# Optimization experiments

Measured on AMD Instinct MI355X. Metric: run time of the kernel, lower is better.

Reference implementation:

```python
import jax, jax.numpy as jnp
import numpy as np
from jax import lax

D_MODEL = 96; D_STATE = 16; D_INNER = 192; DT_RANK = 6; K = 4
BSZ = 2; HH = 64; WW = 64


def setup_inputs() -> dict:
    key = jax.random.key(0)
    ks = jax.random.split(key, 16)
    f = lambda k, shape, s=0.02: (jax.random.normal(k, shape) * s).astype(jnp.float32)
    P = DT_RANK + 2 * D_STATE
    return {
        "x": jax.random.normal(ks[0], (BSZ, HH, WW, D_MODEL), jnp.float32),
        "W_in": f(ks[1], (2 * D_INNER, D_MODEL)),
        "b_in": jnp.zeros((2 * D_INNER,), jnp.float32),
        "conv_w": f(ks[2], (D_INNER, 1, 3, 3)),
        "conv_b": jnp.zeros((D_INNER,), jnp.float32),
        "W_xp": f(ks[3], (K * P, K * D_INNER)),
        "b_xp": jnp.zeros((K * P,), jnp.float32),
        "W_dt": f(ks[4], (K * D_INNER, K * DT_RANK)),
        "b_dt": f(ks[5], (K * D_INNER,), 0.1),
        "A_log": jax.random.normal(ks[6], (K * D_INNER, D_STATE), jnp.float32),
        "D_skip": jnp.ones((K * D_INNER,), jnp.float32),
        "dt_bias": jax.random.normal(ks[7], (K * D_INNER,), jnp.float32),
        "W_out": f(ks[8], (D_MODEL, D_INNER)),
        "b_out": jnp.zeros((D_MODEL,), jnp.float32),
        "gamma": jnp.ones((D_INNER,), jnp.float32),
        "beta": jnp.zeros((D_INNER,), jnp.float32),
    }


def cross_scan(x):
    # x: (B, D, H, W) -> (B, 4, D, L); dirs: row-major, col-major, and their reverses
    B, D, H, W = x.shape
    L = H * W
    x0 = x.reshape(B, D, L)
    x1 = jnp.swapaxes(x, 2, 3).reshape(B, D, L)
    return jnp.stack([x0, x1, x0[..., ::-1], x1[..., ::-1]], axis=1)


def cross_merge(ys):
    # ys: (B, 4, D, H, W) -> (B, D, L); inverse of cross_scan, summed
    B, Kk, D, H, W = ys.shape
    L = H * W
    yf = ys.reshape(B, Kk, D, L)
    y02 = yf[:, 0] + yf[:, 2, :, ::-1]
    y13 = yf[:, 1] + yf[:, 3, :, ::-1]
    y13 = jnp.swapaxes(y13.reshape(B, D, W, H), 2, 3).reshape(B, D, L)
    return y02 + y13


def selective_scan(u, dt, A, Bm, Cm, D_skip, dt_bias):
    # u, dt: (B,K,Dv,L); A: (K,Dv,N); Bm, Cm: (B,K,N,L); D_skip, dt_bias: (K,Dv)
    # NOTE: torch code repeats Bm/Cm across Dv; we broadcast instead (same math).
    dt = jax.nn.softplus(dt + dt_bias[None, :, :, None])
    dt_l = jnp.moveaxis(dt, -1, 0)   # (L,B,K,Dv)
    u_l = jnp.moveaxis(u, -1, 0)     # (L,B,K,Dv)
    B_l = jnp.moveaxis(Bm, -1, 0)    # (L,B,K,N)
    C_l = jnp.moveaxis(Cm, -1, 0)    # (L,B,K,N)

    def step(h, inp):
        dt_t, u_t, b_t, c_t = inp
        dA = jnp.exp(dt_t[..., None] * A[None])                 # (B,K,Dv,N)
        dBu = (dt_t * u_t)[..., None] * b_t[:, :, None, :]      # (B,K,Dv,N)
        h = dA * h + dBu
        y = jnp.einsum('bkdn,bkn->bkd', h, c_t)
        return h, y

    h0 = jnp.zeros(u.shape[:3] + (A.shape[-1],), u.dtype)
    _, ys = lax.scan(step, h0, (dt_l, u_l, B_l, C_l))
    ys = jnp.moveaxis(ys, 0, -1)  # (B,K,Dv,L)
    return ys + u * D_skip[None, :, :, None]


def reference(x, W_in, b_in, conv_w, conv_b, W_xp, b_xp, W_dt, b_dt,
              A_log, D_skip, dt_bias, W_out, b_out, gamma, beta):
    B, H, W, _ = x.shape
    L = H * W
    xz = x @ W_in.T + b_in
    xx, z = jnp.split(xz, 2, axis=-1)
    z = jax.nn.silu(z)
    xc = jnp.transpose(xx, (0, 3, 1, 2))  # (B, D, H, W)
    xc = lax.conv_general_dilated(xc, conv_w, (1, 1), 'SAME',
                                  feature_group_count=D_INNER,
                                  dimension_numbers=('NCHW', 'OIHW', 'NCHW'))
    xc = jax.nn.silu(xc + conv_b[None, :, None, None])

    xs = cross_scan(xc)                      # (B, K, D, L)
    xs_flat = xs.reshape(B, K * D_INNER, L)

    x_dbl = jnp.einsum('bcl,pc->bpl', xs_flat, W_xp) + b_xp[None, :, None]
    x_dbl = x_dbl.reshape(B, K, DT_RANK + 2 * D_STATE, L)
    dts, Bm, Cm = jnp.split(x_dbl, [DT_RANK, DT_RANK + D_STATE], axis=2)
    dts = dts.reshape(B, K * DT_RANK, L)
    dts = jnp.einsum('brl,dr->bdl', dts, W_dt) + b_dt[None, :, None]

    A = -jnp.exp(A_log).reshape(K, D_INNER, D_STATE)
    u = xs_flat.reshape(B, K, D_INNER, L)
    dt = dts.reshape(B, K, D_INNER, L)
    ys = selective_scan(u, dt, A, Bm, Cm,
                        D_skip.reshape(K, D_INNER), dt_bias.reshape(K, D_INNER))

    y = cross_merge(ys.reshape(B, K, D_INNER, H, W))  # (B, D, L)
    y = jnp.transpose(y.reshape(B, D_INNER, H, W), (0, 2, 3, 1))

    mu = jnp.mean(y, axis=-1, keepdims=True)
    var = jnp.mean(jnp.square(y - mu), axis=-1, keepdims=True)
    y = (y - mu) * lax.rsqrt(var + 1e-5) * gamma + beta
    y = y * z
    return y @ W_out.T + b_out
```

## Files before the change

### kernel.cpp

```cpp
#include <hip/hip_runtime.h>
#include <cstdint>
#include <cstddef>


#define CHUNK 16
#define NCK   256

#if __has_builtin(__builtin_amdgcn_exp2f)
#define EXP2(x) __builtin_amdgcn_exp2f(x)
#else
#define EXP2(x) exp2f(x)
#endif
#define LOG2E 1.44269504088896340736f
#define LN2   0.69314718055994530942f

typedef __attribute__((ext_vector_type(8))) short short8;
typedef __attribute__((ext_vector_type(8))) unsigned short ushort8;
typedef __attribute__((ext_vector_type(4))) float f32x4;

__device__ __forceinline__ float siluf(float x){ return x * (1.f/(1.f+__expf(-x))); }
__device__ __forceinline__ float softplus_fast(float v){
  float e  = EXP2(v*LOG2E);
  float sp = LN2*__log2f(1.f + e);
  return (v > 20.f) ? v : sp;
}
__device__ __forceinline__ unsigned short f2b(float f){
  uint32_t u = __float_as_uint(f);
  uint32_t r = (u + 0x7fffu + ((u>>16)&1u)) >> 16;
  return (unsigned short)r;
}
__device__ __forceinline__ short8 cast8(const float* p){
  float4 f0 = *(const float4*)p;
  float4 f1 = *(const float4*)(p+4);
  unsigned short t[8] = {f2b(f0.x),f2b(f0.y),f2b(f0.z),f2b(f0.w),
                         f2b(f1.x),f2b(f1.y),f2b(f1.z),f2b(f1.w)};
  return *(short8*)t;
}

__global__ __launch_bounds__(256) void k_pack(
    const float* __restrict__ Wxp, const float* __restrict__ Win,
    const float* __restrict__ Wout,
    unsigned short* __restrict__ Wf, unsigned short* __restrict__ Wfin,
    unsigned short* __restrict__ Wfout)
{
  int tid = blockIdx.x*256 + threadIdx.x;
  int lane = tid & 63;
  int n = lane & 15, q = lane >> 4;
  if (tid < 18432){
    int rest = tid >> 6;
    int pt = rest % 6; rest /= 6;
    int k32 = rest & 3; rest >>= 2;
    int kc = rest % 6; int ph = rest / 6;
    int p = ph*96 + pt*16 + n;
    int kbase = kc*128 + k32*32 + q*8;
    unsigned short v[8];
#pragma unroll
    for (int j = 0; j < 8; j++)
      v[j] = (p < 152) ? f2b(Wxp[(size_t)p*768 + kbase + j]) : (unsigned short)0;
    *(ushort8*)(Wf + (size_t)tid*8) = *(ushort8*)v;
  } else if (tid < 23040){
    int e = tid - 18432;
    int rest = e >> 6;
    int nt = rest % 24, k32 = rest / 24;
    int p = nt*16 + n;
    int kbase = k32*32 + q*8;
    unsigned short v[8];
#pragma unroll
    for (int j = 0; j < 8; j++) v[j] = f2b(Win[(size_t)p*96 + kbase + j]);
    *(ushort8*)(Wfin + (size_t)e*8) = *(ushort8*)v;
  } else if (tid < 25344){
    int e = tid - 23040;
    int rest = e >> 6;
    int nt = rest % 6, k32 = rest / 6;
    int p = nt*16 + n;
    int kbase = k32*32 + q*8;
    unsigned short v[8];
#pragma unroll
    for (int j = 0; j < 8; j++) v[j] = f2b(Wout[(size_t)p*192 + kbase + j]);
    *(ushort8*)(Wfout + (size_t)e*8) = *(ushort8*)v;
  }
}

__global__ __launch_bounds__(256) void k_gemm_in(
    const float* __restrict__ x, const unsigned short* __restrict__ Wfin,
    const float* __restrict__ bias, float* __restrict__ xx, float* __restrict__ zs)
{
  const int tid = threadIdx.x;
  const int lane = tid & 63, w = tid >> 6;
  const int m0 = blockIdx.x*32;
  const int n = lane & 15, q = lane >> 4;
  f32x4 acc[2][6] = {};
#pragma unroll
  for (int k32 = 0; k32 < 3; k32++){
    int kb = k32*32 + q*8;
    short8 a[2];
#pragma unroll
    for (int mf = 0; mf < 2; mf++)
      a[mf] = cast8(x + (size_t)(m0 + mf*16 + n)*96 + kb);
#pragma unroll
    for (int j = 0; j < 6; j++){
      int nt = w*6 + j;
      short8 bfr = *(const short8*)(Wfin + ((size_t)(k32*24 + nt)*64 + lane)*8);
#pragma unroll
      for (int mf = 0; mf < 2; mf++)
        acc[mf][j] = __builtin_amdgcn_mfma_f32_16x16x32_bf16(a[mf], bfr, acc[mf][j], 0, 0, 0);
    }
  }
#pragma unroll
  for (int mf = 0; mf < 2; mf++)
#pragma unroll
    for (int j = 0; j < 6; j++){
      int nn = w*96 + j*16 + n;
      float bv = bias[nn];
#pragma unroll
      for (int reg = 0; reg < 4; reg++){
        int l = m0 + mf*16 + q*4 + reg;
        float v = acc[mf][j][reg] + bv;
        if (nn < 192) xx[(size_t)l*192 + nn] = v;
        else          zs[(size_t)l*192 + (nn-192)] = siluf(v);
      }
    }
}

__global__ __launch_bounds__(256) void k_conv(
    const float* __restrict__ xx, const float* __restrict__ cw, const float* __restrict__ cb,
    float* __restrict__ xc,
    unsigned short* __restrict__ xcb, unsigned short* __restrict__ xcTb)
{
  int gid = blockIdx.x*256 + threadIdx.x;
  int c = gid % 192;
  int l = (gid/192) & 4095;
  int b = gid / (192*4096);
  int h = l >> 6, w = l & 63;
  float s = 0.f;
#pragma unroll
  for (int kh = 0; kh < 3; kh++){
    int h2 = h + kh - 1;
    if ((unsigned)h2 >= 64u) continue;
#pragma unroll
    for (int kw = 0; kw < 3; kw++){
      int w2 = w + kw - 1;
      if ((unsigned)w2 >= 64u) continue;
      s += xx[((size_t)b*4096 + h2*64 + w2)*192 + c] * cw[c*9 + kh*3 + kw];
    }
  }
  s = siluf(s + cb[c]);
  unsigned short sb = f2b(s);
  size_t i0 = ((size_t)b*4096 + l)*192 + c;
  xc[i0] = s; xcb[i0] = sb;
  int tl = (l & 63)*64 + (l >> 6);
  xcTb[((size_t)b*4096 + tl)*192 + c] = sb;
}

__global__ __launch_bounds__(256) void k_gemm_xdbl(
    const unsigned short* __restrict__ xcb, const unsigned short* __restrict__ xcTb,
    const unsigned short* __restrict__ Wf, const float* __restrict__ bxp,
    float* __restrict__ xdbl, float* __restrict__ dts_c)
{
  __shared__ unsigned short Bsh[4*6*64*8];
  const int tid = threadIdx.x;
  const int lane = tid & 63, w = tid >> 6;
  const int wl = w & 1, wp = w >> 1;
  const int l0 = blockIdx.x*64, ph = blockIdx.y, b = blockIdx.z;
  const int n = lane & 15, q = lane >> 4;
  f32x4 acc[2][3] = {};
  const unsigned short* slab0 = Wf + (size_t)ph*6*12288;
  for (int kc = 0; kc < 6; kc++){
    __syncthreads();
    const ushort8* srcp = (const ushort8*)(slab0 + (size_t)kc*12288);
#pragma unroll
    for (int t = 0; t < 6; t++) ((ushort8*)Bsh)[tid + t*256] = srcp[tid + t*256];
    __syncthreads();
#pragma unroll
    for (int k32 = 0; k32 < 4; k32++){
      int kk = kc*128 + k32*32;
      int dir = kk/192; int ch = kk%192 + q*8;
      const unsigned short* sp = (dir & 1) ? xcTb : xcb;
      bool rev = (dir >= 2);
      short8 a[2];
#pragma unroll
      for (int mt = 0; mt < 2; mt++){
        int ls = l0 + wl*32 + mt*16 + n;
        int row = rev ? 4095 - ls : ls;
        a[mt] = *(const short8*)(sp + ((size_t)b*4096 + row)*192 + ch);
      }
#pragma unroll
      for (int j = 0; j < 3; j++){
        short8 bfr = *(const short8*)&Bsh[((size_t)(k32*6 + wp*3 + j)*64 + lane)*8];
#pragma unroll
        for (int mt = 0; mt < 2; mt++)
          acc[mt][j] = __builtin_amdgcn_mfma_f32_16x16x32_bf16(a[mt], bfr, acc[mt][j], 0, 0, 0);
      }
    }
  }
#pragma unroll
  for (int mt = 0; mt < 2; mt++)
#pragma unroll
    for (int j = 0; j < 3; j++){
      int p = ph*96 + (wp*3+j)*16 + n;
      if (p < 152){
        int k = p/38, pp = p%38;
        int off = (pp < 6) ? pp : pp + 2;
        float bias = bxp[p];
#pragma unroll
        for (int reg = 0; reg < 4; reg++){
          int l = l0 + wl*32 + mt*16 + q*4 + reg;
          float val = acc[mt][j][reg] + bias;
          xdbl[(((size_t)b*4 + k)*4096 + l)*48 + off] = val;
          if (pp < 6) dts_c[((size_t)b*4096 + l)*24 + k*6 + pp] = val;
        }
      }
    }
}

__global__ __launch_bounds__(256) void k_scanA(
    const float* __restrict__ xc, const float* __restrict__ xdbl,
    const float* __restrict__ dts_c,
    const float* __restrict__ A_log, const float* __restrict__ Wdt,
    const float* __restrict__ bdt, const float* __restrict__ dtbias,
    const float* __restrict__ Dskip,
    float* __restrict__ ylcs, float* __restrict__ sdtb, float* __restrict__ Sb)
{
  const int lane = threadIdx.x & 63;
  const int wid  = __builtin_amdgcn_readfirstlane(blockIdx.x*4 + (threadIdx.x >> 6));
  const int ck = wid & (NCK-1); const int g = wid / NCK;
  const int dblk = g % 3; const int bk = g / 3;
  const int k = bk & 3; const int b = bk >> 2;
  const int d = dblk*64 + lane; const int ch = k*192 + d;
  float An[16];
  {
    const float4* ap = (const float4*)(A_log + (size_t)ch*16);
#pragma unroll
    for (int i = 0; i < 4; i++){
      float4 t = ap[i];
      An[4*i+0] = -LOG2E*__expf(t.x); An[4*i+1] = -LOG2E*__expf(t.y);
      An[4*i+2] = -LOG2E*__expf(t.z); An[4*i+3] = -LOG2E*__expf(t.w);
    }
  }
  float Wr[24];
#pragma unroll
  for (int r = 0; r < 24; r++) Wr[r] = Wdt[(size_t)ch*24 + r];
  const float bsum = bdt[ch] + dtbias[ch];
  const float Dv = Dskip[ch];
  const int l0 = ck*CHUNK;
  const bool rev = (k >= 2);
  const int tr = k & 1;
  const int T0 = tr ? ((l0 & 63)*64 + (l0 >> 6)) : l0;
  const int rs = tr ? 64 : 1;
  const int row0 = rev ? 4095 - T0 : T0;
  const int rstep = (rev ? -rs : rs)*192;
  const float* up  = xc + ((size_t)b*4096 + row0)*192 + d;
  const float* qc  = dts_c + ((size_t)b*4096 + l0)*24;
  const float* xbc = xdbl + (((size_t)b*4 + k)*4096 + l0)*48;
  float* ylp = ylcs + ((((size_t)b*4 + k)*4096 + l0)*192 + d)*2;
  float h[16];
#pragma unroll
  for (int n = 0; n < 16; n++) h[n] = 0.f;
  float sdt = 0.f;
#pragma unroll 4
  for (int t = 0; t < CHUNK; t++){
    float u  = up[0];
    float4 B0 = *(const float4*)(xbc + 8);
    float4 B1 = *(const float4*)(xbc + 12);
    float4 B2 = *(const float4*)(xbc + 16);
    float4 B3 = *(const float4*)(xbc + 20);
    float4 C0 = *(const float4*)(xbc + 24);
    float4 C1 = *(const float4*)(xbc + 28);
    float4 C2 = *(const float4*)(xbc + 32);
    float4 C3 = *(const float4*)(xbc + 36);
    float Bv[16] = {B0.x,B0.y,B0.z,B0.w, B1.x,B1.y,B1.z,B1.w,
                    B2.x,B2.y,B2.z,B2.w, B3.x,B3.y,B3.z,B3.w};
    float Cv[16] = {C0.x,C0.y,C0.z,C0.w, C1.x,C1.y,C1.z,C1.w,
                    C2.x,C2.y,C2.z,C2.w, C3.x,C3.y,C3.z,C3.w};
    float4 q0 = *(const float4*)(qc);
    float4 q1 = *(const float4*)(qc + 4);
    float4 q2 = *(const float4*)(qc + 8);
    float4 q3 = *(const float4*)(qc + 12);
    float4 q4 = *(const float4*)(qc + 16);
    float4 q5 = *(const float4*)(qc + 20);
    float qv[24] = {q0.x,q0.y,q0.z,q0.w, q1.x,q1.y,q1.z,q1.w,
                    q2.x,q2.y,q2.z,q2.w, q3.x,q3.y,q3.z,q3.w,
                    q4.x,q4.y,q4.z,q4.w, q5.x,q5.y,q5.z,q5.w};
    float v0 = bsum, v1 = 0.f, v2 = 0.f, v3 = 0.f;
#pragma unroll
    for (int r = 0; r < 24; r += 4){
      v0 = fmaf(Wr[r+0], qv[r+0], v0);
      v1 = fmaf(Wr[r+1], qv[r+1], v1);
      v2 = fmaf(Wr[r+2], qv[r+2], v2);
      v3 = fmaf(Wr[r+3], qv[r+3], v3);
    }
    float dt = softplus_fast((v0+v1) + (v2+v3));
    float dtu = dt*u;
    sdt += dt;
    float y0 = u*Dv;
    float y1 = 0.f;
#pragma unroll
    for (int n = 0; n < 16; n += 2){
      float dA0 = EXP2(dt*An[n]);
      float dA1 = EXP2(dt*An[n+1]);
      h[n]   = fmaf(dA0, h[n],   dtu*Bv[n]);
      h[n+1] = fmaf(dA1, h[n+1], dtu*Bv[n+1]);
      y0 = fmaf(h[n],   Cv[n],   y0);
      y1 = fmaf(h[n+1], Cv[n+1], y1);
    }
    *(float2*)ylp = make_float2(y0 + y1, sdt);
    qc += 24; xbc += 48; up += rstep; ylp += 384;
  }
  size_t base = ((size_t)wid*16)*64 + lane;
  sdtb[(size_t)wid*64 + lane] = sdt;
#pragma unroll
  for (int n = 0; n < 16; n++) Sb[base + n*64] = h[n];
}

__global__ __launch_bounds__(64) void k_scanB(
    const float* __restrict__ A_log, const float* __restrict__ sdtb,
    const float* __restrict__ Sb, float* __restrict__ H0)
{
  int tid = blockIdx.x*64 + threadIdx.x;
  int lane = tid & 63; int n = (tid >> 6) & 15; int g = tid >> 10;
  int dblk = g % 3; int bk = g / 3; int k = bk & 3;
  int ch = k*192 + dblk*64 + lane;
  float An = -LOG2E*__expf(A_log[(size_t)ch*16 + n]);
  float h = 0.f;
#pragma unroll 8
  for (int ck = 0; ck < NCK; ck++){
    size_t sidx = ((size_t)(g*NCK + ck))*64 + lane;
    size_t idx  = (((size_t)(g*NCK + ck)*16) + n)*64 + lane;
    H0[idx] = h;
    h = fmaf(EXP2(An*sdtb[sidx]), h, Sb[idx]);
  }
}

__global__ __launch_bounds__(256) void k_scanC(
    const float* __restrict__ xdbl, const float* __restrict__ A_log,
    const float* __restrict__ ylcs, const float* __restrict__ H0,
    float* __restrict__ ys)
{
  const int lane = threadIdx.x & 63;
  const int wid  = __builtin_amdgcn_readfirstlane(blockIdx.x*4 + (threadIdx.x >> 6));
  const int ck = wid & (NCK-1); const int g = wid / NCK;
  const int dblk = g % 3; const int bk = g / 3;
  const int k = bk & 3; const int b = bk >> 2;
  const int d = dblk*64 + lane; const int ch = k*192 + d;
  float An[16];
  {
    const float4* ap = (const float4*)(A_log + (size_t)ch*16);
#pragma unroll
    for (int i = 0; i < 4; i++){
      float4 t = ap[i];
      An[4*i+0] = -LOG2E*__expf(t.x); An[4*i+1] = -LOG2E*__expf(t.y);
      An[4*i+2] = -LOG2E*__expf(t.z); An[4*i+3] = -LOG2E*__expf(t.w);
    }
  }
  const int l0 = ck*CHUNK;
  const bool rev = (k >= 2);
  const int tr = k & 1;
  const int T0 = tr ? ((l0 & 63)*64 + (l0 >> 6)) : l0;
  const int rs = tr ? 64 : 1;
  const int row0 = rev ? 4095 - T0 : T0;
  const int rstep = (rev ? -rs : rs)*192;
  const float* xbc = xdbl + (((size_t)b*4 + k)*4096 + l0)*48;
  const float* ylp = ylcs + ((((size_t)b*4 + k)*4096 + l0)*192 + d)*2;
  float* ysp = ys + ((size_t)(k*2 + b))*4096*192 + (size_t)row0*192 + d;
  float h0r[16];
  size_t base = ((size_t)wid*16)*64 + lane;
#pragma unroll
  for (int n = 0; n < 16; n++) h0r[n] = H0[base + n*64];
#pragma unroll 4
  for (int t = 0; t < CHUNK; t++){
    float2 yc = *(const float2*)ylp;
    float4 C0 = *(const float4*)(xbc + 24);
    float4 C1 = *(const float4*)(xbc + 28);
    float4 C2 = *(const float4*)(xbc + 32);
    float4 C3 = *(const float4*)(xbc + 36);
    float Cv[16] = {C0.x,C0.y,C0.z,C0.w, C1.x,C1.y,C1.z,C1.w,
                    C2.x,C2.y,C2.z,C2.w, C3.x,C3.y,C3.z,C3.w};
    float cs = yc.y;
    float y0 = yc.x, y1 = 0.f;
#pragma unroll
    for (int n = 0; n < 16; n += 2){
      float e0 = EXP2(An[n]*cs)   * h0r[n];
      float e1 = EXP2(An[n+1]*cs) * h0r[n+1];
      y0 = fmaf(Cv[n],   e0, y0);
      y1 = fmaf(Cv[n+1], e1, y1);
    }
    ysp[0] = y0 + y1;
    ylp += 384; xbc += 48; ysp += rstep;
  }
}

__global__ __launch_bounds__(256) void k_lngemm(
    const float* __restrict__ ys, const float* __restrict__ zs,
    const float* __restrict__ gamma, const float* __restrict__ beta,
    const unsigned short* __restrict__ Wfout, const float* __restrict__ bout,
    float* __restrict__ out)
{
  __shared__ unsigned short Ash[32*200];
  const int tid = threadIdx.x;
  {
    const int row_l = tid >> 3, o = tid & 7;
    const int row = blockIdx.x*32 + row_l;
    const int b = row >> 12, l = row & 4095;
    const int c0 = o*24;
    float s[24];
#pragma unroll
    for (int j = 0; j < 6; j++){
      float sx = 0.f, sy = 0.f, sz = 0.f, sw = 0.f;
#pragma unroll
      for (int k = 0; k < 4; k++){
        float4 t = *(const float4*)(ys + (((size_t)(k*2+b))*4096 + l)*192 + c0 + j*4);
        sx += t.x; sy += t.y; sz += t.z; sw += t.w;
      }
      s[j*4+0]=sx; s[j*4+1]=sy; s[j*4+2]=sz; s[j*4+3]=sw;
    }
    float tot = 0.f;
#pragma unroll
    for (int j = 0; j < 24; j++) tot += s[j];
#pragma unroll
    for (int off = 1; off < 8; off <<= 1) tot += __shfl_xor(tot, off);
    float mean = tot*(1.f/192.f);
    float vs = 0.f;
#pragma unroll
    for (int j = 0; j < 24; j++){ s[j] -= mean; vs = fmaf(s[j], s[j], vs); }
#pragma unroll
    for (int off = 1; off < 8; off <<= 1) vs += __shfl_xor(vs, off);
    float rstd = rsqrtf(vs*(1.f/192.f) + 1e-5f);
    unsigned short vb[24];
#pragma unroll
    for (int j = 0; j < 6; j++){
      float4 g4 = *(const float4*)(gamma + c0 + j*4);
      float4 b4 = *(const float4*)(beta  + c0 + j*4);
      float4 z4 = *(const float4*)(zs + (size_t)row*192 + c0 + j*4);
      vb[j*4+0] = f2b((s[j*4+0]*rstd*g4.x + b4.x)*z4.x);
      vb[j*4+1] = f2b((s[j*4+1]*rstd*g4.y + b4.y)*z4.y);
      vb[j*4+2] = f2b((s[j*4+2]*rstd*g4.z + b4.z)*z4.z);
      vb[j*4+3] = f2b((s[j*4+3]*rstd*g4.w + b4.w)*z4.w);
    }
#pragma unroll
    for (int j = 0; j < 3; j++)
      *(ushort8*)(Ash + row_l*200 + c0 + j*8) = *(ushort8*)(vb + j*8);
  }
  __syncthreads();
  const int lane = tid & 63, w = tid >> 6;
  const int wm = w & 1, wn = w >> 1;
  const int n = lane & 15, q = lane >> 4;
  const int m0 = blockIdx.x*32 + wm*16;
  f32x4 acc[3] = {};
#pragma unroll
  for (int k32 = 0; k32 < 6; k32++){
    int kb = k32*32 + q*8;
    short8 a = *(const short8*)(Ash + (wm*16 + n)*200 + kb);
#pragma unroll
    for (int j = 0; j < 3; j++){
      int nt = wn*3 + j;
      short8 bfr = *(const short8*)(Wfout + ((size_t)(k32*6 + nt)*64 + lane)*8);
      acc[j] = __builtin_amdgcn_mfma_f32_16x16x32_bf16(a, bfr, acc[j], 0, 0, 0);
    }
  }
#pragma unroll
  for (int j = 0; j < 3; j++){
    int nn = wn*48 + j*16 + n;
    float bv = bout[nn];
#pragma unroll
    for (int reg = 0; reg < 4; reg++){
      int m = m0 + q*4 + reg;
      out[(size_t)m*96 + nn] = acc[j][reg] + bv;
    }
  }
}

extern "C" void kernel_launch(void* const* d_in, const int* in_sizes, int n_in,
                              void* d_out, int out_size, void* d_ws, size_t ws_size,
                              hipStream_t stream)
{
  const float* x      = (const float*)d_in[0];
  const float* W_in   = (const float*)d_in[1];
  const float* b_in   = (const float*)d_in[2];
  const float* conv_w = (const float*)d_in[3];
  const float* conv_b = (const float*)d_in[4];
  const float* W_xp   = (const float*)d_in[5];
  const float* b_xp   = (const float*)d_in[6];
  const float* W_dt   = (const float*)d_in[7];
  const float* b_dt   = (const float*)d_in[8];
  const float* A_log  = (const float*)d_in[9];
  const float* D_skip = (const float*)d_in[10];
  const float* dt_bias= (const float*)d_in[11];
  const float* W_out  = (const float*)d_in[12];
  const float* b_out  = (const float*)d_in[13];
  const float* gamma  = (const float*)d_in[14];
  const float* beta   = (const float*)d_in[15];
  float* out = (float*)d_out;

  float* ws    = (float*)d_ws;
  float* xx    = ws;
  float* zs    = ws + 1572864;
  float* xc    = ws + 3145728;
  float* xdbl  = ws + 4718592;
  float* ysb   = ws + 6291456;
  float* Sb    = ws + 12582912;
  float* H0    = ws + 18874368;
  float* sdtb  = ws + 25165824;
  float* dts_c = ws + 25559040;
  float* ylcs  = ws + 25755648;
  unsigned short* xcb   = (unsigned short*)(ws + 38338560);
  unsigned short* xcTb  = xcb + 1572864;
  unsigned short* Wf    = (unsigned short*)(ws + 39911424);
  unsigned short* Wfin  = (unsigned short*)(ws + 39985152);
  unsigned short* Wfout = (unsigned short*)(ws + 40003584);

  k_pack     <<<99,             256, 0, stream>>>(W_xp, W_in, W_out, Wf, Wfin, Wfout);
  k_gemm_in  <<<256,            256, 0, stream>>>(x, Wfin, b_in, xx, zs);
  k_conv     <<<6144,           256, 0, stream>>>(xx, conv_w, conv_b, xc, xcb, xcTb);
  k_gemm_xdbl<<<dim3(64, 2, 2), 256, 0, stream>>>(xcb, xcTb, Wf, b_xp, xdbl, dts_c);
  k_scanA    <<<1536,           256, 0, stream>>>(xc, xdbl, dts_c, A_log, W_dt, b_dt, dt_bias, D_skip, ylcs, sdtb, Sb);
  k_scanB    <<<384,            64,  0, stream>>>(A_log, sdtb, Sb, H0);
  k_scanC    <<<1536,           256, 0, stream>>>(xdbl, A_log, ylcs, H0, ysb);
  k_lngemm   <<<256,            256, 0, stream>>>(ysb, zs, gamma, beta, Wfout, b_out, out);
}
```

Baseline: 207.3 us.

## Split chunk-state scan into two-level span scan, vectorize conv, halve xdbl tile

The serial 256-step carry scan over chunk states becomes a two-level scan. First, 8 spans of 32 chunks are scanned in parallel, recording local prefix states and cumulative dt. Then a short 8-step pass over span totals runs, and scanC combines the two with exp(A*cum_dt). The depthwise conv now processes 4 channels per thread with float4 loads and vector stores. The xdbl GEMM tile shrinks to 32 rows for more blocks. The scan change trades a long serial dependency for an extra kernel launch and extra workspace traffic.

```diff
diff --git a/kernel.cpp b/kernel.cpp
--- a/kernel.cpp
+++ b/kernel.cpp
@@ -5,6 +5,8 @@
 
 #define CHUNK 16
 #define NCK   256
+#define SPAN  32
+#define NSP   8
 
 #if __has_builtin(__builtin_amdgcn_exp2f)
 #define EXP2(x) __builtin_amdgcn_exp2f(x)
@@ -128,11 +130,11 @@
     unsigned short* __restrict__ xcb, unsigned short* __restrict__ xcTb)
 {
   int gid = blockIdx.x*256 + threadIdx.x;
-  int c = gid % 192;
-  int l = (gid/192) & 4095;
-  int b = gid / (192*4096);
+  int c4 = gid % 48; int c = c4*4;
+  int l = (gid/48) & 4095;
+  int b = gid / (48*4096);
   int h = l >> 6, w = l & 63;
-  float s = 0.f;
+  float sx = 0.f, sy = 0.f, sz = 0.f, sw = 0.f;
 #pragma unroll
   for (int kh = 0; kh < 3; kh++){
     int h2 = h + kh - 1;
@@ -141,15 +143,24 @@
     for (int kw = 0; kw < 3; kw++){
       int w2 = w + kw - 1;
       if ((unsigned)w2 >= 64u) continue;
-      s += xx[((size_t)b*4096 + h2*64 + w2)*192 + c] * cw[c*9 + kh*3 + kw];
-    }
-  }
-  s = siluf(s + cb[c]);
-  unsigned short sb = f2b(s);
+      float4 v = *(const float4*)(xx + ((size_t)b*4096 + h2*64 + w2)*192 + c);
+      int o = kh*3 + kw;
+      sx = fmaf(v.x, cw[(c+0)*9 + o], sx);
+      sy = fmaf(v.y, cw[(c+1)*9 + o], sy);
+      sz = fmaf(v.z, cw[(c+2)*9 + o], sz);
+      sw = fmaf(v.w, cw[(c+3)*9 + o], sw);
+    }
+  }
+  float4 cbv = *(const float4*)(cb + c);
+  float4 s;
+  s.x = siluf(sx + cbv.x); s.y = siluf(sy + cbv.y);
+  s.z = siluf(sz + cbv.z); s.w = siluf(sw + cbv.w);
+  unsigned short sb[4] = {f2b(s.x), f2b(s.y), f2b(s.z), f2b(s.w)};
   size_t i0 = ((size_t)b*4096 + l)*192 + c;
-  xc[i0] = s; xcb[i0] = sb;
+  *(float4*)(xc + i0) = s;
+  *(uint2*)(xcb + i0) = *(uint2*)sb;
   int tl = (l & 63)*64 + (l >> 6);
-  xcTb[((size_t)b*4096 + tl)*192 + c] = sb;
+  *(uint2*)(xcTb + ((size_t)b*4096 + tl)*192 + c) = *(uint2*)sb;
 }
 
 __global__ __launch_bounds__(256) void k_gemm_xdbl(
@@ -161,9 +172,9 @@
   const int tid = threadIdx.x;
   const int lane = tid & 63, w = tid >> 6;
   const int wl = w & 1, wp = w >> 1;
-  const int l0 = blockIdx.x*64, ph = blockIdx.y, b = blockIdx.z;
+  const int l0 = blockIdx.x*32, ph = blockIdx.y, b = blockIdx.z;
   const int n = lane & 15, q = lane >> 4;
-  f32x4 acc[2][3] = {};
+  f32x4 acc[3] = {};
   const unsigned short* slab0 = Wf + (size_t)ph*6*12288;
   for (int kc = 0; kc < 6; kc++){
     __syncthreads();
@@ -177,40 +188,32 @@
       int dir = kk/192; int ch = kk%192 + q*8;
       const unsigned short* sp = (dir & 1) ? xcTb : xcb;
       bool rev = (dir >= 2);
-      short8 a[2];
-#pragma unroll
-      for (int mt = 0; mt < 2; mt++){
-        int ls = l0 + wl*32 + mt*16 + n;
-        int row = rev ? 4095 - ls : ls;
-        a[mt] = *(const short8*)(sp + ((size_t)b*4096 + row)*192 + ch);
-      }
+      int ls = l0 + wl*16 + n;
+      int row = rev ? 4095 - ls : ls;
+      short8 a = *(const short8*)(sp + ((size_t)b*4096 + row)*192 + ch);
 #pragma unroll
       for (int j = 0; j < 3; j++){
         short8 bfr = *(const short8*)&Bsh[((size_t)(k32*6 + wp*3 + j)*64 + lane)*8];
-#pragma unroll
-        for (int mt = 0; mt < 2; mt++)
-          acc[mt][j] = __builtin_amdgcn_mfma_f32_16x16x32_bf16(a[mt], bfr, acc[mt][j], 0, 0, 0);
+        acc[j] = __builtin_amdgcn_mfma_f32_16x16x32_bf16(a, bfr, acc[j], 0, 0, 0);
       }
     }
   }
 #pragma unroll
-  for (int mt = 0; mt < 2; mt++)
-#pragma unroll
-    for (int j = 0; j < 3; j++){
-      int p = ph*96 + (wp*3+j)*16 + n;
-      if (p < 152){
-        int k = p/38, pp = p%38;
-        int off = (pp < 6) ? pp : pp + 2;
-        float bias = bxp[p];
-#pragma unroll
-        for (int reg = 0; reg < 4; reg++){
-          int l = l0 + wl*32 + mt*16 + q*4 + reg;
-          float val = acc[mt][j][reg] + bias;
-          xdbl[(((size_t)b*4 + k)*4096 + l)*48 + off] = val;
-          if (pp < 6) dts_c[((size_t)b*4096 + l)*24 + k*6 + pp] = val;
-        }
+  for (int j = 0; j < 3; j++){
+    int p = ph*96 + (wp*3+j)*16 + n;
+    if (p < 152){
+      int k = p/38, pp = p%38;
+      int off = (pp < 6) ? pp : pp + 2;
+      float bias = bxp[p];
+#pragma unroll
+      for (int reg = 0; reg < 4; reg++){
+        int l = l0 + wl*16 + q*4 + reg;
+        float val = acc[j][reg] + bias;
+        xdbl[(((size_t)b*4 + k)*4096 + l)*48 + off] = val;
+        if (pp < 6) dts_c[((size_t)b*4096 + l)*24 + k*6 + pp] = val;
       }
     }
+  }
 }
 
 __global__ __launch_bounds__(256) void k_scanA(
@@ -312,9 +315,38 @@
   for (int n = 0; n < 16; n++) Sb[base + n*64] = h[n];
 }
 
-__global__ __launch_bounds__(64) void k_scanB(
+__global__ __launch_bounds__(256) void k_scanB1(
     const float* __restrict__ A_log, const float* __restrict__ sdtb,
-    const float* __restrict__ Sb, float* __restrict__ H0)
+    const float* __restrict__ Sb,
+    float* __restrict__ H0loc, float* __restrict__ cloc,
+    float* __restrict__ SpanS, float* __restrict__ SpanC)
+{
+  int tid = blockIdx.x*256 + threadIdx.x;
+  int lane = tid & 63; int n = (tid >> 6) & 15;
+  int span = (tid >> 10) & (NSP-1); int g = tid >> 13;
+  int dblk = g % 3; int bk = g / 3; int k = bk & 3;
+  int ch = k*192 + dblk*64 + lane;
+  float An = -LOG2E*__expf(A_log[(size_t)ch*16 + n]);
+  float h = 0.f, cs = 0.f;
+  int wid0 = g*NCK + span*SPAN;
+#pragma unroll 8
+  for (int c = 0; c < SPAN; c++){
+    size_t sidx = ((size_t)(wid0 + c))*64 + lane;
+    size_t idx  = (((size_t)(wid0 + c)*16) + n)*64 + lane;
+    H0loc[idx] = h;
+    if (n == 0) cloc[sidx] = cs;
+    float sd = sdtb[sidx];
+    h = fmaf(EXP2(An*sd), h, Sb[idx]);
+    cs += sd;
+  }
+  size_t sp = (size_t)(g*NSP + span);
+  SpanS[(sp*16 + n)*64 + lane] = h;
+  if (n == 0) SpanC[sp*64 + lane] = cs;
+}
+
+__global__ __launch_bounds__(64) void k_scanB2(
+    const float* __restrict__ A_log, const float* __restrict__ SpanS,
+    const float* __restrict__ SpanC, float* __restrict__ H0span)
 {
   int tid = blockIdx.x*64 + threadIdx.x;
   int lane = tid & 63; int n = (tid >> 6) & 15; int g = tid >> 10;
@@ -322,18 +354,20 @@
   int ch = k*192 + dblk*64 + lane;
   float An = -LOG2E*__expf(A_log[(size_t)ch*16 + n]);
   float h = 0.f;
-#pragma unroll 8
-  for (int ck = 0; ck < NCK; ck++){
-    size_t sidx = ((size_t)(g*NCK + ck))*64 + lane;
-    size_t idx  = (((size_t)(g*NCK + ck)*16) + n)*64 + lane;
-    H0[idx] = h;
-    h = fmaf(EXP2(An*sdtb[sidx]), h, Sb[idx]);
+#pragma unroll
+  for (int span = 0; span < NSP; span++){
+    size_t sp = (size_t)(g*NSP + span);
+    size_t idx = (sp*16 + n)*64 + lane;
+    H0span[idx] = h;
+    h = fmaf(EXP2(An*SpanC[sp*64 + lane]), h, SpanS[idx]);
   }
 }
 
 __global__ __launch_bounds__(256) void k_scanC(
     const float* __restrict__ xdbl, const float* __restrict__ A_log,
-    const float* __restrict__ ylcs, const float* __restrict__ H0,
+    const float* __restrict__ ylcs,
+    const float* __restrict__ H0loc, const float* __restrict__ cloc,
+    const float* __restrict__ H0span,
     float* __restrict__ ys)
 {
   const int lane = threadIdx.x & 63;
@@ -363,9 +397,16 @@
   const float* ylp = ylcs + ((((size_t)b*4 + k)*4096 + l0)*192 + d)*2;
   float* ysp = ys + ((size_t)(k*2 + b))*4096*192 + (size_t)row0*192 + d;
   float h0r[16];
-  size_t base = ((size_t)wid*16)*64 + lane;
-#pragma unroll
-  for (int n = 0; n < 16; n++) h0r[n] = H0[base + n*64];
+  {
+    size_t base = ((size_t)wid*16)*64 + lane;
+    float cl = cloc[(size_t)wid*64 + lane];
+    size_t sp = (size_t)(g*NSP + (ck >> 5));
+#pragma unroll
+    for (int n = 0; n < 16; n++){
+      float hs = H0span[(sp*16 + n)*64 + lane];
+      h0r[n] = fmaf(EXP2(An[n]*cl), hs, H0loc[base + n*64]);
+    }
+  }
 #pragma unroll 4
   for (int t = 0; t < CHUNK; t++){
     float2 yc = *(const float2*)ylp;
@@ -491,29 +532,34 @@
   const float* beta   = (const float*)d_in[15];
   float* out = (float*)d_out;
 
-  float* ws    = (float*)d_ws;
-  float* xx    = ws;
-  float* zs    = ws + 1572864;
-  float* xc    = ws + 3145728;
-  float* xdbl  = ws + 4718592;
-  float* ysb   = ws + 6291456;
-  float* Sb    = ws + 12582912;
-  float* H0    = ws + 18874368;
-  float* sdtb  = ws + 25165824;
-  float* dts_c = ws + 25559040;
-  float* ylcs  = ws + 25755648;
-  unsigned short* xcb   = (unsigned short*)(ws + 38338560);
+  float* ws     = (float*)d_ws;
+  float* xx     = ws;
+  float* zs     = ws + 1572864;
+  float* xc     = ws + 3145728;
+  float* xdbl   = ws + 4718592;
+  float* ysb    = ws + 6291456;
+  float* Sb     = ws + 12582912;
+  float* H0loc  = ws + 18874368;
+  float* sdtb   = ws + 25165824;
+  float* dts_c  = ws + 25559040;
+  float* ylcs   = ws + 25755648;
+  float* cloc   = ws + 38338560;
+  float* SpanS  = ws + 38731776;
+  float* SpanC  = ws + 38928384;
+  float* H0span = ws + 38940672;
+  unsigned short* xcb   = (unsigned short*)(ws + 39137280);
   unsigned short* xcTb  = xcb + 1572864;
-  unsigned short* Wf    = (unsigned short*)(ws + 39911424);
-  unsigned short* Wfin  = (unsigned short*)(ws + 39985152);
-  unsigned short* Wfout = (unsigned short*)(ws + 40003584);
-
-  k_pack     <<<99,             256, 0, stream>>>(W_xp, W_in, W_out, Wf, Wfin, Wfout);
-  k_gemm_in  <<<256,            256, 0, stream>>>(x, Wfin, b_in, xx, zs);
-  k_conv     <<<6144,           256, 0, stream>>>(xx, conv_w, conv_b, xc, xcb, xcTb);
-  k_gemm_xdbl<<<dim3(64, 2, 2), 256, 0, stream>>>(xcb, xcTb, Wf, b_xp, xdbl, dts_c);
-  k_scanA    <<<1536,           256, 0, stream>>>(xc, xdbl, dts_c, A_log, W_dt, b_dt, dt_bias, D_skip, ylcs, sdtb, Sb);
-  k_scanB    <<<384,            64,  0, stream>>>(A_log, sdtb, Sb, H0);
-  k_scanC    <<<1536,           256, 0, stream>>>(xdbl, A_log, ylcs, H0, ysb);
-  k_lngemm   <<<256,            256, 0, stream>>>(ysb, zs, gamma, beta, Wfout, b_out, out);
-}
+  unsigned short* Wf    = (unsigned short*)(ws + 40710144);
+  unsigned short* Wfin  = (unsigned short*)(ws + 40783872);
+  unsigned short* Wfout = (unsigned short*)(ws + 40802304);
+
+  k_pack     <<<99,              256, 0, stream>>>(W_xp, W_in, W_out, Wf, Wfin, Wfout);
+  k_gemm_in  <<<256,             256, 0, stream>>>(x, Wfin, b_in, xx, zs);
+  k_conv     <<<1536,            256, 0, stream>>>(xx, conv_w, conv_b, xc, xcb, xcTb);
+  k_gemm_xdbl<<<dim3(128, 2, 2), 256, 0, stream>>>(xcb, xcTb, Wf, b_xp, xdbl, dts_c);
+  k_scanA    <<<1536,            256, 0, stream>>>(xc, xdbl, dts_c, A_log, W_dt, b_dt, dt_bias, D_skip, ylcs, sdtb, Sb);
+  k_scanB1   <<<768,             256, 0, stream>>>(A_log, sdtb, Sb, H0loc, cloc, SpanS, SpanC);
+  k_scanB2   <<<384,             64,  0, stream>>>(A_log, SpanS, SpanC, H0span);
+  k_scanC    <<<1536,            256, 0, stream>>>(xdbl, A_log, ylcs, H0loc, cloc, H0span, ysb);
+  k_lngemm   <<<256,             256, 0, stream>>>(ysb, zs, gamma, beta, Wfout, b_out, out);
+}
```

Measured after the change: 210.1 us. About the same (+1.4%).
